# Kernel optimization log

Hardware: AMD Instinct MI355X
Metric: run time of the kernel (lower is better)

The kernel has to match this reference:

```python
import jax, jax.numpy as jnp
import numpy as np

D_MODEL = 1024
N_HEADS = 16
HEAD_DIM = D_MODEL // N_HEADS
D_FF = 4 * D_MODEL
SEQ = 2048
BATCH = 2
EPS = 1e-6


def setup_inputs() -> dict:
    key = jax.random.key(0)
    ks = jax.random.split(key, 8)
    s = 0.02
    return {
        "x": jax.random.normal(ks[0], (SEQ, BATCH, D_MODEL), dtype=jnp.float32),
        "g1": jnp.ones((D_MODEL,), dtype=jnp.float32),                # norm1 weight
        "g2": jnp.ones((D_MODEL,), dtype=jnp.float32),                # norm2 weight
        "Wq": jax.random.normal(ks[1], (N_HEADS, D_MODEL, HEAD_DIM), dtype=jnp.float32) * s,
        "Wk": jax.random.normal(ks[2], (N_HEADS, D_MODEL, HEAD_DIM), dtype=jnp.float32) * s,
        "Wv": jax.random.normal(ks[3], (N_HEADS, D_MODEL, HEAD_DIM), dtype=jnp.float32) * s,
        "Wo": jax.random.normal(ks[4], (D_MODEL, D_MODEL), dtype=jnp.float32) * s,
        "W1": jax.random.normal(ks[5], (D_MODEL, D_FF), dtype=jnp.float32) * s,
        "W2": jax.random.normal(ks[6], (D_FF, D_MODEL), dtype=jnp.float32) * s,
    }


def _rmsnorm(x, g):
    rms = jnp.sqrt(jnp.mean(x * x, axis=-1, keepdims=True) + EPS)
    return g * (x / rms)


def _block(x, g1, g2, Wq, Wk, Wv, Wo, W1, W2):
    S = x.shape[0]
    scale = HEAD_DIM ** -0.5
    # --- attention (pre-norm) ---
    h = _rmsnorm(x, g1)                              # (S, B, D)
    Q = jnp.einsum('sbd,hdk->bhsk', h, Wq)           # (B, H, S, K)
    K = jnp.einsum('sbd,hdk->bhsk', h, Wk)
    V = jnp.einsum('sbd,hdk->bhsk', h, Wv)
    scores = jnp.einsum('bhsk,bhtk->bhst', Q, K) * scale
    causal = jnp.tril(jnp.ones((S, S), dtype=bool))
    scores = jnp.where(causal, scores, -jnp.inf)
    attn = jax.nn.softmax(scores, axis=-1)
    ctx = jnp.einsum('bhst,bhtk->sbhk', attn, V)     # heads concatenated in order
    ctx = ctx.reshape(S, x.shape[1], D_MODEL)
    x = x + ctx @ Wo
    # --- FFN (pre-norm) ---
    h2 = _rmsnorm(x, g2)
    x = x + jax.nn.silu(h2 @ W1) @ W2
    return x


def reference(x, g1, g2, Wq, Wk, Wv, Wo, W1, W2):
    return _block(x, g1, g2, Wq, Wk, Wv, Wo, W1, W2)
```

## Files before the change

### kernel.cpp

```cpp
#include <hip/hip_runtime.h>

typedef unsigned short u16;
typedef __bf16 bf16x8 __attribute__((ext_vector_type(8)));
typedef u16 u16x8 __attribute__((ext_vector_type(8)));
typedef u16 u16x4 __attribute__((ext_vector_type(4)));
typedef float f32x4 __attribute__((ext_vector_type(4)));

__device__ __forceinline__ u16 f2bf(float f) {
    union { float f; unsigned int u; } x; x.f = f;
    unsigned int r = x.u + 0x7FFFu + ((x.u >> 16) & 1u);
    return (u16)(r >> 16);
}

__device__ __forceinline__ u16 f2bf_hw(float f) {
    union { __bf16 b; u16 u; } x; x.b = (__bf16)f; return x.u;
}

__device__ __forceinline__ void gload_lds16(const u16* g, u16* l) {
    __builtin_amdgcn_global_load_lds(
        (const __attribute__((address_space(1))) unsigned int*)g,
        (__attribute__((address_space(3))) unsigned int*)l, 16, 0, 0);
}


__global__ __launch_bounds__(256) void qkvT_k(
    const float* __restrict__ Wq, const float* __restrict__ Wk,
    const float* __restrict__ Wv, u16* __restrict__ out)
{
    __shared__ float T[64][65];
    const int d0 = blockIdx.x * 64;
    const int y = blockIdx.y;
    const int wsel = y >> 4, h = y & 15;
    const float* W = (wsel == 0) ? Wq : (wsel == 1) ? Wk : Wv;
    const float scale = (wsel == 0) ? 0.125f * 1.44269504088896f : 1.0f;
    const int tid = threadIdx.x;
    const int tr = tid >> 4;
    const int tc = (tid & 15) * 4;
    #pragma unroll
    for (int k = 0; k < 4; k++) {
        f32x4 v = *(const f32x4*)(W + (size_t)h * 65536 + (size_t)(d0 + 16 * k + tr) * 64 + tc);
        T[16 * k + tr][tc]     = v[0];
        T[16 * k + tr][tc + 1] = v[1];
        T[16 * k + tr][tc + 2] = v[2];
        T[16 * k + tr][tc + 3] = v[3];
    }
    __syncthreads();
    #pragma unroll
    for (int k = 0; k < 4; k++) {
        const int kk = 16 * k + tr;
        u16x4 o;
        #pragma unroll
        for (int i = 0; i < 4; i++) o[i] = f2bf(T[tc + i][kk] * scale);
        *(u16x4*)(out + (size_t)(wsel * 1024 + h * 64 + kk) * 1024 + d0 + tc) = o;
    }
}

__global__ __launch_bounds__(256) void transT_k(
    const float* __restrict__ in, u16* __restrict__ out, int R, int C)
{
    __shared__ float T[64][65];
    const int r0 = blockIdx.x * 64, c0 = blockIdx.y * 64;
    const int tid = threadIdx.x;
    const int tr = tid >> 4;
    const int tc = (tid & 15) * 4;
    #pragma unroll
    for (int k = 0; k < 4; k++) {
        f32x4 v = *(const f32x4*)(in + (size_t)(c0 + 16 * k + tr) * R + r0 + tc);
        T[16 * k + tr][tc]     = v[0];
        T[16 * k + tr][tc + 1] = v[1];
        T[16 * k + tr][tc + 2] = v[2];
        T[16 * k + tr][tc + 3] = v[3];
    }
    __syncthreads();
    #pragma unroll
    for (int k = 0; k < 4; k++) {
        const int rl = 16 * k + tr;
        u16x4 o;
        #pragma unroll
        for (int i = 0; i < 4; i++) o[i] = f2bf(T[tc + i][rl]);
        *(u16x4*)(out + (size_t)(r0 + rl) * C + c0 + tc) = o;
    }
}

__global__ __launch_bounds__(256) void vtrans_k(const u16* __restrict__ qkv, u16* __restrict__ vT)
{
    __shared__ u16 T[64][72];
    const int bh = blockIdx.x, b = bh >> 4, h = bh & 15;
    const int s0 = blockIdx.y * 64;
    const int tid = threadIdx.x;
    const int r = tid >> 2, c0 = (tid & 3) * 16;
    const u16* src = qkv + ((size_t)((s0 + r) * 2 + b)) * 3072 + 2048 + h * 64 + c0;
    *(u16x8*)&T[r][c0] = *(const u16x8*)src;
    *(u16x8*)&T[r][c0 + 8] = *(const u16x8*)(src + 8);
    __syncthreads();
    u16x8 o0, o1;
    #pragma unroll
    for (int i = 0; i < 8; i++) o0[i] = T[c0 + i][r];
    #pragma unroll
    for (int i = 0; i < 8; i++) o1[i] = T[c0 + 8 + i][r];
    u16* dst = vT + (size_t)(bh * 64 + r) * 2048 + s0 + c0;
    *(u16x8*)dst = o0;
    *(u16x8*)(dst + 8) = o1;
}

__global__ __launch_bounds__(256) void rmsnorm_k(
    const float* __restrict__ x, const float* __restrict__ g, u16* __restrict__ out)
{
    const int row = blockIdx.x;
    const int tid = threadIdx.x;
    const float* xr = x + (size_t)row * 1024;
    f32x4 v = *(const f32x4*)(xr + tid * 4);
    float ss = v[0] * v[0] + v[1] * v[1] + v[2] * v[2] + v[3] * v[3];
    #pragma unroll
    for (int off = 32; off > 0; off >>= 1) ss += __shfl_down(ss, off);
    __shared__ float red[4];
    if ((tid & 63) == 0) red[tid >> 6] = ss;
    __syncthreads();
    float sum = red[0] + red[1] + red[2] + red[3];
    float rinv = rsqrtf(sum * (1.0f / 1024.0f) + 1e-6f);
    f32x4 gv = *(const f32x4*)(g + tid * 4);
    u16x4 o;
    #pragma unroll
    for (int i = 0; i < 4; i++) o[i] = f2bf(v[i] * gv[i] * rinv);
    *(u16x4*)(out + (size_t)row * 1024 + tid * 4) = o;
}

__global__ __launch_bounds__(256) void addred_norm_k(
    const float* __restrict__ res, const float* __restrict__ p0,
    const float* __restrict__ p1, const float* __restrict__ g,
    float* __restrict__ xout, u16* __restrict__ hout)
{
    const int row = blockIdx.x;
    const int tid = threadIdx.x;
    const size_t base = (size_t)row * 1024 + tid * 4;
    f32x4 a = *(const f32x4*)(res + base);
    f32x4 b = *(const f32x4*)(p0 + base);
    f32x4 c = *(const f32x4*)(p1 + base);
    f32x4 o = a + b + c;
    *(f32x4*)(xout + base) = o;
    float ss = o[0] * o[0] + o[1] * o[1] + o[2] * o[2] + o[3] * o[3];
    #pragma unroll
    for (int off = 32; off > 0; off >>= 1) ss += __shfl_down(ss, off);
    __shared__ float red[4];
    if ((tid & 63) == 0) red[tid >> 6] = ss;
    __syncthreads();
    float sum = red[0] + red[1] + red[2] + red[3];
    float rinv = rsqrtf(sum * (1.0f / 1024.0f) + 1e-6f);
    f32x4 gv = *(const f32x4*)(g + tid * 4);
    u16x4 hv;
    #pragma unroll
    for (int i = 0; i < 4; i++) hv[i] = f2bf(o[i] * gv[i] * rinv);
    *(u16x4*)(hout + base) = hv;
}

__global__ __launch_bounds__(256) void addred4_k(
    const float* __restrict__ xm, const float* __restrict__ a0,
    const float* __restrict__ a1, const float* __restrict__ a2,
    const float* __restrict__ a3, float* __restrict__ out)
{
    int i = (blockIdx.x * 256 + threadIdx.x) * 4;
    f32x4 v = *(const f32x4*)(xm + i);
    v = v + *(const f32x4*)(a0 + i);
    v = v + *(const f32x4*)(a1 + i);
    v = v + *(const f32x4*)(a2 + i);
    v = v + *(const f32x4*)(a3 + i);
    *(f32x4*)(out + i) = v;
}

template <int MODE>
__global__ __launch_bounds__(256) void gemm_bt_k(
    const u16* __restrict__ A, const u16* __restrict__ BT,
    u16* __restrict__ outB, float* __restrict__ outF, const float* __restrict__ res,
    int M, int N, int K, int klen)
{
    __shared__ u16 As[2][128 * 64];
    __shared__ u16 Bs[2][128 * 64];
    const int tid = threadIdx.x;
    const int lane = tid & 63, w = tid >> 6;
    const int wm = w >> 1, wn = w & 1;
    const int quad = lane >> 4, l15 = lane & 15;
    const int bid = blockIdx.x + gridDim.x * blockIdx.y;
    const int bj = bid >> 3;
    const int m0 = ((bid & 7) * 4 + (bj & 3)) * 128;
    const int n0 = (bj >> 2) * 128;
    const int kbeg = blockIdx.z * klen;

    f32x4 acc[4][4] = {};

    const int srow = (w << 3) + (lane >> 3);
    const int swz = ((lane & 7) ^ (lane >> 3)) << 3;
    const u16* aA = A + (size_t)(m0 + srow) * K + kbeg + swz;
    const u16* aB = BT + (size_t)(n0 + srow) * K + kbeg + swz;
    const int wo = w * 512;
    const int rsw = (l15 & 7) << 3;

    #pragma unroll
    for (int c = 0; c < 4; c++) {
        gload_lds16(aA + (size_t)(c * 32) * K, &As[0][0] + c * 2048 + wo);
        gload_lds16(aB + (size_t)(c * 32) * K, &Bs[0][0] + c * 2048 + wo);
    }

    int cur = 0;
    for (int k0 = 0; k0 < klen; k0 += 64) {
        __syncthreads();
        if (k0 + 64 < klen) {
            #pragma unroll
            for (int c = 0; c < 4; c++) {
                gload_lds16(aA + (size_t)(c * 32) * K + k0 + 64, &As[cur ^ 1][0] + c * 2048 + wo);
                gload_lds16(aB + (size_t)(c * 32) * K + k0 + 64, &Bs[cur ^ 1][0] + c * 2048 + wo);
            }
        }
        const u16* AB = &As[cur][0];
        const u16* BB = &Bs[cur][0];
        #pragma unroll
        for (int kh = 0; kh < 2; kh++) {
            const int cb = ((kh * 4 + quad) << 3);
            bf16x8 af[4], bfr[4];
            #pragma unroll
            for (int i = 0; i < 4; i++)
                af[i] = *(const bf16x8*)(AB + (wm * 64 + i * 16 + l15) * 64 + (cb ^ rsw));
            #pragma unroll
            for (int j = 0; j < 4; j++)
                bfr[j] = *(const bf16x8*)(BB + (wn * 64 + j * 16 + l15) * 64 + (cb ^ rsw));
            #pragma unroll
            for (int i = 0; i < 4; i++)
                #pragma unroll
                for (int j = 0; j < 4; j++)
                    acc[i][j] = __builtin_amdgcn_mfma_f32_16x16x32_bf16(af[i], bfr[j], acc[i][j], 0, 0, 0);
        }
        cur ^= 1;
    }

    float* outFz = (MODE == 3) ? outF + (size_t)blockIdx.z * M * N : outF;
    #pragma unroll
    for (int i = 0; i < 4; i++) {
        const int row = m0 + wm * 64 + i * 16 + quad * 4;
        #pragma unroll
        for (int j = 0; j < 4; j++) {
            const int col = n0 + wn * 64 + j * 16 + l15;
            #pragma unroll
            for (int r = 0; r < 4; r++) {
                const size_t idx = (size_t)(row + r) * N + col;
                float v = acc[i][j][r];
                if (MODE == 0) {
                    outB[idx] = f2bf_hw(v);
                } else if (MODE == 1) {
                    outF[idx] = res[idx] + v;
                } else if (MODE == 2) {
                    float e = exp2f(v * -1.44269504088896f);
                    outB[idx] = f2bf_hw(v * __builtin_amdgcn_rcpf(1.0f + e));
                } else {
                    outFz[idx] = v;
                }
            }
        }
    }
}

#define MM8(FH) \
    { _Pragma("unroll") \
      for (int i_ = 0; i_ < 4; i_++) { \
        acc[(FH)*4+i_][0] = __builtin_amdgcn_mfma_f32_16x16x32_bf16(a[i_], b0, acc[(FH)*4+i_][0], 0, 0, 0); \
        acc[(FH)*4+i_][1] = __builtin_amdgcn_mfma_f32_16x16x32_bf16(a[i_], b1, acc[(FH)*4+i_][1], 0, 0, 0); \
        acc[(FH)*4+i_][2] = __builtin_amdgcn_mfma_f32_16x16x32_bf16(a[i_], b2, acc[(FH)*4+i_][2], 0, 0, 0); \
        acc[(FH)*4+i_][3] = __builtin_amdgcn_mfma_f32_16x16x32_bf16(a[i_], b3, acc[(FH)*4+i_][3], 0, 0, 0); \
      } }

template <int MODE>
__global__ __launch_bounds__(512, 2) void gemm8p_k(
    const u16* __restrict__ A, const u16* __restrict__ BT,
    u16* __restrict__ outB, float* __restrict__ q0, float* __restrict__ q1,
    float* __restrict__ q2, float* __restrict__ q3,
    int N, int K, int klen)
{
    __shared__ u16 sm[65536];
    const int tid = threadIdx.x;
    const int lane = tid & 63, w = tid >> 6;
    const int l15 = lane & 15, quad = lane >> 4;
    const int wm = w >> 2, wn = w & 3;

    const int nwg = gridDim.x;
    const int bid = blockIdx.x;
    const int s = (bid & 7) * (nwg >> 3) + (bid >> 3);
    const int m0 = (s & 15) * 256;
    const int n0 = (s >> 4) * 256;
    const int kbeg = blockIdx.z * klen;
    const int nT = klen >> 6;

    const int srow = w * 16 + (lane >> 2);
    const int scol = (((lane & 3) ^ ((lane >> 3) & 3)) << 3);
    const u16* gA = A + (size_t)(m0 + srow) * K + kbeg + scol;
    const u16* gB = BT + (size_t)(n0 + srow) * K + kbeg + scol;
    const size_t cstep = (size_t)128 * K;

    const int rswz = ((quad ^ ((l15 >> 1) & 3)) << 3);
    const int raoff = (wm * 128 + l15) * 32 + rswz;
    const int rboff = (wn * 64 + l15) * 32 + rswz;

    f32x4 acc[8][4] = {};

    auto stA = [&](int t, int kh) {
        u16* d = sm + (t & 1) * 32768 + kh * 8192 + w * 512;
        const u16* g = gA + (size_t)(t * 64 + kh * 32);
        gload_lds16(g, d);
        gload_lds16(g + cstep, d + 4096);
    };
    auto stB = [&](int t, int kh) {
        u16* d = sm + (t & 1) * 32768 + 16384 + kh * 8192 + w * 512;
        const u16* g = gB + (size_t)(t * 64 + kh * 32);
        gload_lds16(g, d);
        gload_lds16(g + cstep, d + 4096);
    };
    bf16x8 b0, b1, b2, b3;
    auto rdB = [&](int buf, int kh) {
        const u16* p = sm + buf * 32768 + 16384 + kh * 8192 + rboff;
        b0 = *(const bf16x8*)(p);
        b1 = *(const bf16x8*)(p + 512);
        b2 = *(const bf16x8*)(p + 1024);
        b3 = *(const bf16x8*)(p + 1536);
    };
    auto rdA = [&](int buf, int kh, int fh, bf16x8* a) {
        const u16* p = sm + buf * 32768 + kh * 8192 + fh * 2048 + raoff;
        a[0] = *(const bf16x8*)(p);
        a[1] = *(const bf16x8*)(p + 512);
        a[2] = *(const bf16x8*)(p + 1024);
        a[3] = *(const bf16x8*)(p + 1536);
    };

    stA(0, 0); stB(0, 0); stA(0, 1); stB(0, 1);
    if (nT > 1) {
        stA(1, 0); stB(1, 0);
        asm volatile("s_waitcnt vmcnt(4)" ::: "memory");
    } else {
        asm volatile("s_waitcnt vmcnt(0)" ::: "memory");
    }
    __builtin_amdgcn_s_barrier();

    for (int t = 0; t < nT; t++) {
        const int buf = t & 1;
        bf16x8 a[4];
        rdA(buf, 0, 0, a); rdB(buf, 0);
        if (t + 1 < nT) stA(t + 1, 1);
        __builtin_amdgcn_s_barrier();
        asm volatile("s_waitcnt lgkmcnt(0)" ::: "memory");
        __builtin_amdgcn_sched_barrier(0);
        __builtin_amdgcn_s_setprio(1);
        MM8(0)
        __builtin_amdgcn_s_setprio(0);
        __builtin_amdgcn_s_barrier();
        rdA(buf, 0, 1, a);
        if (t + 1 < nT) stB(t + 1, 1);
        __builtin_amdgcn_s_barrier();
        asm volatile("s_waitcnt lgkmcnt(0)" ::: "memory");
        __builtin_amdgcn_sched_barrier(0);
        __builtin_amdgcn_s_setprio(1);
        MM8(1)
        __builtin_amdgcn_s_setprio(0);
        __builtin_amdgcn_s_barrier();
        rdA(buf, 1, 0, a); rdB(buf, 1);
        if (t + 2 < nT) stA(t + 2, 0);
        __builtin_amdgcn_s_barrier();
        asm volatile("s_waitcnt lgkmcnt(0)" ::: "memory");
        __builtin_amdgcn_sched_barrier(0);
        __builtin_amdgcn_s_setprio(1);
        MM8(0)
        __builtin_amdgcn_s_setprio(0);
        __builtin_amdgcn_s_barrier();
        rdA(buf, 1, 1, a);
        if (t + 2 < nT) {
            stB(t + 2, 0);
            asm volatile("s_waitcnt vmcnt(4)" ::: "memory");
        } else {
            asm volatile("s_waitcnt vmcnt(0)" ::: "memory");
        }
        __builtin_amdgcn_s_barrier();
        asm volatile("s_waitcnt lgkmcnt(0)" ::: "memory");
        __builtin_amdgcn_sched_barrier(0);
        __builtin_amdgcn_s_setprio(1);
        MM8(1)
        __builtin_amdgcn_s_setprio(0);
        __builtin_amdgcn_s_barrier();
    }

    float* po = nullptr;
    if (MODE == 3)
        po = (blockIdx.z == 0) ? q0 : (blockIdx.z == 1) ? q1 : (blockIdx.z == 2) ? q2 : q3;
    #pragma unroll
    for (int mf = 0; mf < 8; mf++) {
        const int row = m0 + wm * 128 + mf * 16 + quad * 4;
        #pragma unroll
        for (int nf = 0; nf < 4; nf++) {
            const int col = n0 + wn * 64 + nf * 16 + l15;
            #pragma unroll
            for (int r = 0; r < 4; r++) {
                const size_t idx = (size_t)(row + r) * N + col;
                const float v = acc[mf][nf][r];
                if (MODE == 0) {
                    outB[idx] = f2bf_hw(v);
                } else if (MODE == 2) {
                    float e = exp2f(v * -1.44269504088896f);
                    outB[idx] = f2bf_hw(v * __builtin_amdgcn_rcpf(1.0f + e));
                } else {
                    po[idx] = v;
                }
            }
        }
    }
}

__global__ __launch_bounds__(256) void attn_k(const u16* __restrict__ qkv,
                                              const u16* __restrict__ vT,
                                              u16* __restrict__ ctx)
{
    const int bh = blockIdx.x;
    const int qt = 31 - (int)blockIdx.y;
    const int b = bh >> 4, h = bh & 15;
    const int q0 = qt * 64;
    const int tid = threadIdx.x;
    const int lane = tid & 63, w = tid >> 6;
    const int quad = lane >> 4, l15 = lane & 15;

    __shared__ u16 QP[64][72];
    __shared__ u16 Ks[2][4096];
    __shared__ u16 Vs[2][4096];

    {
        const int r = tid >> 2, c0 = (tid & 3) * 16;
        const u16* src = qkv + ((size_t)((q0 + r) * 2 + b)) * 3072 + h * 64 + c0;
        *(u16x8*)&QP[r][c0] = *(const u16x8*)(src);
        *(u16x8*)&QP[r][c0 + 8] = *(const u16x8*)(src + 8);
    }
    __syncthreads();

    const bf16x8 aq0 = *(const bf16x8*)&QP[16 * w + l15][quad * 8];
    const bf16x8 aq1 = *(const bf16x8*)&QP[16 * w + l15][32 + quad * 8];

    bf16x8 ones;
    #pragma unroll
    for (int i = 0; i < 8; i++) ones[i] = (__bf16)1.0f;

    const int kr = (w << 3) + (lane >> 3);
    const int swz = ((lane & 7) ^ (lane >> 3)) << 3;
    const int ldsoff = w * 512;
    const u16* kbase0 = qkv + ((size_t)(kr * 2 + b)) * 3072 + 1024 + h * 64 + swz;
    const u16* kbase1 = kbase0 + (size_t)32 * 2 * 3072;
    const u16* vrow0 = vT + (size_t)(bh * 64 + kr) * 2048 + swz;
    const u16* vrow1 = vrow0 + (size_t)32 * 2048;

    const int rsw = (l15 & 7) << 3;

    f32x4 o[4] = {};
    f32x4 accl = {};

    gload_lds16(kbase0, &Ks[0][0] + ldsoff);
    gload_lds16(kbase1, &Ks[0][0] + 2048 + ldsoff);
    gload_lds16(vrow0, &Vs[0][0] + ldsoff);
    gload_lds16(vrow1, &Vs[0][0] + 2048 + ldsoff);

    int cur = 0;
    for (int t0 = 0; t0 <= q0; t0 += 64) {
        __syncthreads();
        if (t0 + 64 <= q0) {
            const size_t go = (size_t)(t0 + 64) * 2 * 3072;
            u16* KB = &Ks[cur ^ 1][0];
            u16* VB = &Vs[cur ^ 1][0];
            gload_lds16(kbase0 + go, KB + ldsoff);
            gload_lds16(kbase1 + go, KB + 2048 + ldsoff);
            gload_lds16(vrow0 + (t0 + 64), VB + ldsoff);
            gload_lds16(vrow1 + (t0 + 64), VB + 2048 + ldsoff);
        }
        const u16* KB = &Ks[cur][0];
        const u16* VB = &Vs[cur][0];

        f32x4 s[4];
        #pragma unroll
        for (int j = 0; j < 4; j++) {
            const u16* kb = KB + (j * 16 + l15) * 64;
            bf16x8 bk0 = *(const bf16x8*)(kb + (((quad << 3) ^ rsw)));
            bf16x8 bk1 = *(const bf16x8*)(kb + ((((quad + 4) << 3) ^ rsw)));
            f32x4 c = {};
            c = __builtin_amdgcn_mfma_f32_16x16x32_bf16(aq0, bk0, c, 0, 0, 0);
            c = __builtin_amdgcn_mfma_f32_16x16x32_bf16(aq1, bk1, c, 0, 0, 0);
            s[j] = c;
        }

        if (t0 == q0) {
            #pragma unroll
            for (int j = 0; j < 4; j++)
                #pragma unroll
                for (int r = 0; r < 4; r++)
                    if ((j * 16 + l15) > (16 * w + quad * 4 + r)) s[j][r] = -1e30f;
        }

        #pragma unroll
        for (int j = 0; j < 4; j++)
            #pragma unroll
            for (int r = 0; r < 4; r++)
                QP[16 * w + quad * 4 + r][j * 16 + l15] = f2bf_hw(exp2f(s[j][r]));

        bf16x8 ap0 = *(const bf16x8*)&QP[16 * w + l15][quad * 8];
        bf16x8 ap1 = *(const bf16x8*)&QP[16 * w + l15][32 + quad * 8];
        accl = __builtin_amdgcn_mfma_f32_16x16x32_bf16(ap0, ones, accl, 0, 0, 0);
        accl = __builtin_amdgcn_mfma_f32_16x16x32_bf16(ap1, ones, accl, 0, 0, 0);
        #pragma unroll
        for (int j = 0; j < 4; j++) {
            const u16* vb = VB + (j * 16 + l15) * 64;
            bf16x8 bv0 = *(const bf16x8*)(vb + (((quad << 3) ^ rsw)));
            bf16x8 bv1 = *(const bf16x8*)(vb + ((((quad + 4) << 3) ^ rsw)));
            o[j] = __builtin_amdgcn_mfma_f32_16x16x32_bf16(ap0, bv0, o[j], 0, 0, 0);
            o[j] = __builtin_amdgcn_mfma_f32_16x16x32_bf16(ap1, bv1, o[j], 0, 0, 0);
        }
        cur ^= 1;
    }

    f32x4 linv;
    #pragma unroll
    for (int r = 0; r < 4; r++) linv[r] = 1.0f / accl[r];
    #pragma unroll
    for (int j = 0; j < 4; j++)
        #pragma unroll
        for (int r = 0; r < 4; r++) {
            int q = q0 + 16 * w + quad * 4 + r;
            int col = h * 64 + j * 16 + l15;
            ctx[((size_t)q * 2 + b) * 1024 + col] = f2bf_hw(o[j][r] * linv[r]);
        }
}

extern "C" void kernel_launch(void* const* d_in, const int* in_sizes, int n_in,
                              void* d_out, int out_size, void* d_ws, size_t ws_size,
                              hipStream_t stream)
{
    (void)in_sizes; (void)n_in; (void)out_size; (void)ws_size;
    const float* x  = (const float*)d_in[0];
    const float* g1 = (const float*)d_in[1];
    const float* g2 = (const float*)d_in[2];
    const float* Wq = (const float*)d_in[3];
    const float* Wk = (const float*)d_in[4];
    const float* Wv = (const float*)d_in[5];
    const float* Wo = (const float*)d_in[6];
    const float* W1 = (const float*)d_in[7];
    const float* W2 = (const float*)d_in[8];
    float* out = (float*)d_out;

    char* ws = (char*)d_ws;
    u16*   bqkvT = (u16*)(ws);
    u16*   woT   = (u16*)(ws + 6291456);
    u16*   w1T   = (u16*)(ws + 8388608);
    u16*   w2T   = (u16*)(ws + 16777216);
    u16*   h1    = (u16*)(ws + 25165824);
    u16*   qkvB  = (u16*)(ws + 33554432);
    u16*   vT    = (u16*)(ws + 25165824);
    u16*   ctxB  = (u16*)(ws + 58720256);
    float* xmid  = (float*)(ws + 41943040);
    u16*   h2    = (u16*)(ws + 83886080);
    u16*   actB  = (u16*)(ws + 92274688);
    float* partO = (float*)(ws + 92274688);
    float* p0 = (float*)(ws);
    float* p1 = (float*)(ws + 25165824);
    float* p2 = (float*)(ws + 58720256);
    float* p3 = (float*)(ws + 75497472);

    qkvT_k<<<dim3(16, 48), 256, 0, stream>>>(Wq, Wk, Wv, bqkvT);
    transT_k<<<dim3(16, 16), 256, 0, stream>>>(Wo, woT, 1024, 1024);
    transT_k<<<dim3(64, 16), 256, 0, stream>>>(W1, w1T, 4096, 1024);
    transT_k<<<dim3(16, 64), 256, 0, stream>>>(W2, w2T, 1024, 4096);

    rmsnorm_k<<<4096, 256, 0, stream>>>(x, g1, h1);

    gemm8p_k<0><<<dim3(192, 1, 1), 512, 0, stream>>>(h1, bqkvT, qkvB,
                                                     nullptr, nullptr, nullptr, nullptr,
                                                     3072, 1024, 1024);
    vtrans_k<<<dim3(32, 32), 256, 0, stream>>>(qkvB, vT);
    attn_k<<<dim3(32, 32), 256, 0, stream>>>(qkvB, vT, ctxB);

    gemm_bt_k<3><<<dim3(8, 32, 2), 256, 0, stream>>>(ctxB, woT, nullptr, partO, nullptr,
                                                     4096, 1024, 1024, 512);
    addred_norm_k<<<4096, 256, 0, stream>>>(x, partO, partO + 4096 * 1024, g2, xmid, h2);

    gemm8p_k<2><<<dim3(256, 1, 1), 512, 0, stream>>>(h2, w1T, actB,
                                                     nullptr, nullptr, nullptr, nullptr,
                                                     4096, 1024, 1024);
    gemm8p_k<3><<<dim3(64, 1, 4), 512, 0, stream>>>(actB, w2T, nullptr,
                                                    p0, p1, p2, p3,
                                                    1024, 4096, 1024);
    addred4_k<<<4096 * 1024 / 1024, 256, 0, stream>>>(xmid, p0, p1, p2, p3, out);
}
```

Before: 330.7 us.

## Transpose attention MFMAs to keep P in registers via permlane swap

The attention kernel now computes S^T = K·Q^T so each lane holds scores for its own query row. The exp'd probabilities are packed to bf16 with v_cvt_pk_bf16_f32 and rearranged across lanes with v_permlane32_swap, so they feed the PV MFMA directly instead of round-tripping through the QP shared buffer. Q is loaded straight from global, the QP LDS array and its barrier are removed, launch bounds request 4 blocks per CU, s_setprio is raised around MFMA sections, and output stores become 4-wide vectors. This relies on carefully permuted K row indices and inline asm correctness.

```diff
diff --git a/kernel.cpp b/kernel.cpp
--- a/kernel.cpp
+++ b/kernel.cpp
@@ -408,9 +408,9 @@
     }
 }
 
-__global__ __launch_bounds__(256) void attn_k(const u16* __restrict__ qkv,
-                                              const u16* __restrict__ vT,
-                                              u16* __restrict__ ctx)
+__global__ __launch_bounds__(256, 4) void attn_k(const u16* __restrict__ qkv,
+                                                 const u16* __restrict__ vT,
+                                                 u16* __restrict__ ctx)
 {
     const int bh = blockIdx.x;
     const int qt = 31 - (int)blockIdx.y;
@@ -420,20 +420,13 @@
     const int lane = tid & 63, w = tid >> 6;
     const int quad = lane >> 4, l15 = lane & 15;
 
-    __shared__ u16 QP[64][72];
     __shared__ u16 Ks[2][4096];
     __shared__ u16 Vs[2][4096];
 
-    {
-        const int r = tid >> 2, c0 = (tid & 3) * 16;
-        const u16* src = qkv + ((size_t)((q0 + r) * 2 + b)) * 3072 + h * 64 + c0;
-        *(u16x8*)&QP[r][c0] = *(const u16x8*)(src);
-        *(u16x8*)&QP[r][c0 + 8] = *(const u16x8*)(src + 8);
-    }
-    __syncthreads();
-
-    const bf16x8 aq0 = *(const bf16x8*)&QP[16 * w + l15][quad * 8];
-    const bf16x8 aq1 = *(const bf16x8*)&QP[16 * w + l15][32 + quad * 8];
+    const int q = q0 + 16 * w + l15;
+    const u16* qrow = qkv + ((size_t)(q * 2 + b)) * 3072 + h * 64;
+    const bf16x8 aq0 = *(const bf16x8*)(qrow + quad * 8);
+    const bf16x8 aq1 = *(const bf16x8*)(qrow + 32 + quad * 8);
 
     bf16x8 ones;
     #pragma unroll
@@ -447,7 +440,11 @@
     const u16* vrow0 = vT + (size_t)(bh * 64 + kr) * 2048 + swz;
     const u16* vrow1 = vrow0 + (size_t)32 * 2048;
 
-    const int rsw = (l15 & 7) << 3;
+    const int sl = (l15 & 3) | ((l15 & 4) << 1) | ((l15 & 8) >> 1);
+    const int rswk = (sl & 7) << 3;
+    const int rswv = (l15 & 7) << 3;
+    const int sq = ((quad & 1) << 1) | (quad >> 1);
+    const int qloc = 16 * w + l15;
 
     f32x4 o[4] = {};
     f32x4 accl = {};
@@ -473,57 +470,72 @@
         const u16* VB = &Vs[cur][0];
 
         f32x4 s[4];
-        #pragma unroll
-        for (int j = 0; j < 4; j++) {
-            const u16* kb = KB + (j * 16 + l15) * 64;
-            bf16x8 bk0 = *(const bf16x8*)(kb + (((quad << 3) ^ rsw)));
-            bf16x8 bk1 = *(const bf16x8*)(kb + ((((quad + 4) << 3) ^ rsw)));
+        __builtin_amdgcn_s_setprio(1);
+        #pragma unroll
+        for (int tg = 0; tg < 4; tg++) {
+            const u16* kb = KB + (16 * tg + sl) * 64;
+            bf16x8 ak0 = *(const bf16x8*)(kb + ((quad << 3) ^ rswk));
+            bf16x8 ak1 = *(const bf16x8*)(kb + (((quad + 4) << 3) ^ rswk));
             f32x4 c = {};
-            c = __builtin_amdgcn_mfma_f32_16x16x32_bf16(aq0, bk0, c, 0, 0, 0);
-            c = __builtin_amdgcn_mfma_f32_16x16x32_bf16(aq1, bk1, c, 0, 0, 0);
-            s[j] = c;
-        }
+            c = __builtin_amdgcn_mfma_f32_16x16x32_bf16(ak0, aq0, c, 0, 0, 0);
+            c = __builtin_amdgcn_mfma_f32_16x16x32_bf16(ak1, aq1, c, 0, 0, 0);
+            s[tg] = c;
+        }
+        __builtin_amdgcn_s_setprio(0);
 
         if (t0 == q0) {
             #pragma unroll
-            for (int j = 0; j < 4; j++)
+            for (int tg = 0; tg < 4; tg++)
                 #pragma unroll
                 for (int r = 0; r < 4; r++)
-                    if ((j * 16 + l15) > (16 * w + quad * 4 + r)) s[j][r] = -1e30f;
-        }
-
-        #pragma unroll
-        for (int j = 0; j < 4; j++)
-            #pragma unroll
-            for (int r = 0; r < 4; r++)
-                QP[16 * w + quad * 4 + r][j * 16 + l15] = f2bf_hw(exp2f(s[j][r]));
-
-        bf16x8 ap0 = *(const bf16x8*)&QP[16 * w + l15][quad * 8];
-        bf16x8 ap1 = *(const bf16x8*)&QP[16 * w + l15][32 + quad * 8];
-        accl = __builtin_amdgcn_mfma_f32_16x16x32_bf16(ap0, ones, accl, 0, 0, 0);
-        accl = __builtin_amdgcn_mfma_f32_16x16x32_bf16(ap1, ones, accl, 0, 0, 0);
-        #pragma unroll
-        for (int j = 0; j < 4; j++) {
-            const u16* vb = VB + (j * 16 + l15) * 64;
-            bf16x8 bv0 = *(const bf16x8*)(vb + (((quad << 3) ^ rsw)));
-            bf16x8 bv1 = *(const bf16x8*)(vb + ((((quad + 4) << 3) ^ rsw)));
-            o[j] = __builtin_amdgcn_mfma_f32_16x16x32_bf16(ap0, bv0, o[j], 0, 0, 0);
-            o[j] = __builtin_amdgcn_mfma_f32_16x16x32_bf16(ap1, bv1, o[j], 0, 0, 0);
-        }
+                    if ((16 * tg + 4 * sq + r) > qloc) s[tg][r] = -1e30f;
+        }
+
+        unsigned dd[4][2];
+        #pragma unroll
+        for (int tg = 0; tg < 4; tg++) {
+            float e0 = exp2f(s[tg][0]), e1 = exp2f(s[tg][1]);
+            float e2 = exp2f(s[tg][2]), e3 = exp2f(s[tg][3]);
+            asm("v_cvt_pk_bf16_f32 %0, %1, %2" : "=v"(dd[tg][0]) : "v"(e0), "v"(e1));
+            asm("v_cvt_pk_bf16_f32 %0, %1, %2" : "=v"(dd[tg][1]) : "v"(e2), "v"(e3));
+        }
+        unsigned x0 = dd[0][0], y0 = dd[1][0];
+        asm volatile("v_permlane32_swap_b32 %0, %1" : "+v"(x0), "+v"(y0));
+        unsigned x1 = dd[0][1], y1 = dd[1][1];
+        asm volatile("v_permlane32_swap_b32 %0, %1" : "+v"(x1), "+v"(y1));
+        unsigned x2 = dd[2][0], y2 = dd[3][0];
+        asm volatile("v_permlane32_swap_b32 %0, %1" : "+v"(x2), "+v"(y2));
+        unsigned x3 = dd[2][1], y3 = dd[3][1];
+        asm volatile("v_permlane32_swap_b32 %0, %1" : "+v"(x3), "+v"(y3));
+
+        union { unsigned u[4]; bf16x8 v; } pu0, pu1;
+        pu0.u[0] = x0; pu0.u[1] = x1; pu0.u[2] = y0; pu0.u[3] = y1;
+        pu1.u[0] = x2; pu1.u[1] = x3; pu1.u[2] = y2; pu1.u[3] = y3;
+        const bf16x8 pf0 = pu0.v, pf1 = pu1.v;
+
+        __builtin_amdgcn_s_setprio(1);
+        accl = __builtin_amdgcn_mfma_f32_16x16x32_bf16(ones, pf0, accl, 0, 0, 0);
+        accl = __builtin_amdgcn_mfma_f32_16x16x32_bf16(ones, pf1, accl, 0, 0, 0);
+        #pragma unroll
+        for (int i = 0; i < 4; i++) {
+            const u16* vb = VB + (i * 16 + l15) * 64;
+            bf16x8 av0 = *(const bf16x8*)(vb + ((quad << 3) ^ rswv));
+            bf16x8 av1 = *(const bf16x8*)(vb + (((quad + 4) << 3) ^ rswv));
+            o[i] = __builtin_amdgcn_mfma_f32_16x16x32_bf16(av0, pf0, o[i], 0, 0, 0);
+            o[i] = __builtin_amdgcn_mfma_f32_16x16x32_bf16(av1, pf1, o[i], 0, 0, 0);
+        }
+        __builtin_amdgcn_s_setprio(0);
         cur ^= 1;
     }
 
-    f32x4 linv;
-    #pragma unroll
-    for (int r = 0; r < 4; r++) linv[r] = 1.0f / accl[r];
-    #pragma unroll
-    for (int j = 0; j < 4; j++)
-        #pragma unroll
-        for (int r = 0; r < 4; r++) {
-            int q = q0 + 16 * w + quad * 4 + r;
-            int col = h * 64 + j * 16 + l15;
-            ctx[((size_t)q * 2 + b) * 1024 + col] = f2bf_hw(o[j][r] * linv[r]);
-        }
+    const float linv = 1.0f / accl[0];
+    #pragma unroll
+    for (int i = 0; i < 4; i++) {
+        u16x4 ov;
+        #pragma unroll
+        for (int r = 0; r < 4; r++) ov[r] = f2bf_hw(o[i][r] * linv);
+        *(u16x4*)(ctx + ((size_t)(q * 2 + b)) * 1024 + h * 64 + i * 16 + quad * 4) = ov;
+    }
 }
 
 extern "C" void kernel_launch(void* const* d_in, const int* in_sizes, int n_in,
```

After: 321.0 us. -2.9%, faster.
